# Kernel tuning notes

Measured on AMD Instinct MI355X. Metric: run time of the kernel, lower is better.

## Reference

```python
import jax, jax.numpy as jnp
import numpy as np

WINDOW_SIZE = 11
CHANNEL = 3
SIGMA = 1.5
C1 = 0.01 ** 2
C2 = 0.03 ** 2


def _create_window(window_size: int, channel: int) -> jnp.ndarray:
    coords = jnp.arange(window_size, dtype=jnp.float32) - window_size // 2
    g = jnp.exp(-coords ** 2 / (2 * SIGMA ** 2))
    g = g / g.sum()
    w2d = jnp.outer(g, g)  # [K, K]
    # depthwise conv kernel, OIHW with O=channel, I=1
    return jnp.broadcast_to(w2d, (channel, 1, window_size, window_size))


def _depthwise_conv(x, window):
    pad = WINDOW_SIZE // 2
    return jax.lax.conv_general_dilated(
        x, window,
        window_strides=(1, 1),
        padding=[(pad, pad), (pad, pad)],
        dimension_numbers=("NCHW", "OIHW", "NCHW"),
        feature_group_count=x.shape[1],
    )


def setup_inputs() -> dict:
    key = jax.random.key(0)
    k1, k2 = jax.random.split(key)
    pred = jax.random.uniform(k1, (16, 3, 512, 512), dtype=jnp.float32)
    target = jax.random.uniform(k2, (16, 3, 512, 512), dtype=jnp.float32)
    window = _create_window(WINDOW_SIZE, CHANNEL)
    return {"pred": pred, "target": target, "window": window}


def reference(pred, target, window):
    mu1 = _depthwise_conv(pred, window)
    mu2 = _depthwise_conv(target, window)
    mu1_sq = mu1 * mu1
    mu2_sq = mu2 * mu2
    mu1_mu2 = mu1 * mu2
    sigma1_sq = _depthwise_conv(pred * pred, window) - mu1_sq
    sigma2_sq = _depthwise_conv(target * target, window) - mu2_sq
    sigma12 = _depthwise_conv(pred * target, window) - mu1_mu2
    ssim_map = ((2 * mu1_mu2 + C1) * (2 * sigma12 + C2)) / (
        (mu1_sq + mu2_sq + C1) * (sigma1_sq + sigma2_sq + C2)
    )
    return 1.0 - ssim_map.mean()
```

## Files before the change

kernel.cpp:

```cpp
#include <hip/hip_runtime.h>

#define IMG_H 512
#define IMG_W 512
#define IMG_N (IMG_H * IMG_W)
#define NPLANES 48
#define TILE 64
#define XS 80
#define SSIM_C1 0.0001f
#define SSIM_C2 0.0009f

typedef _Float16 f16x2 __attribute__((ext_vector_type(2)));
typedef _Float16 f16x4 __attribute__((ext_vector_type(4)));
typedef _Float16 f16x8 __attribute__((ext_vector_type(8)));
typedef float    f32x4 __attribute__((ext_vector_type(4)));

__device__ __forceinline__ unsigned pk2(float a, float b) {
    return __builtin_bit_cast(unsigned,
        __builtin_amdgcn_cvt_pkrtz(a, b));
}
__device__ __forceinline__ f16x2 pk2h(float a, float b) {
    return __builtin_bit_cast(f16x2, __builtin_amdgcn_cvt_pkrtz(a, b));
}

template <bool CHECK>
__device__ __forceinline__ void stage_inputs(
    const float* __restrict__ pp, const float* __restrict__ tp,
    unsigned short* Xp, unsigned short* Xt,
    const int tid, const int base_r, const int base_c)
{
    float4   pb[7], tb[7];
    unsigned offv[7];
    bool     okv[7];
    #pragma unroll
    for (int i = 0; i < 7; ++i) {
        unsigned fi = (unsigned)tid + 256u * i;
        if (i == 6) fi = (fi < 1600u) ? fi : 0u;
        const unsigned ri = fi / 20u;
        const unsigned q  = fi - 20u * ri;
        int gr = base_r - 8 + (int)ri;
        int gc = base_c - 8 + 4 * (int)q;
        bool ok = true;
        if (CHECK) {
            ok = ((unsigned)gr < (unsigned)IMG_H) && ((unsigned)gc < (unsigned)IMG_W);
            gr = min(max(gr, 0), IMG_H - 1);
            gc = min(max(gc, 0), IMG_W - 4);
        }
        const int idx = gr * IMG_W + gc;
        pb[i]   = *(const float4*)(pp + idx);
        tb[i]   = *(const float4*)(tp + idx);
        okv[i]  = ok;
        offv[i] = ri * XS + 4u * q;
    }
    #pragma unroll
    for (int i = 0; i < 7; ++i) {
        float4 p4 = pb[i], t4 = tb[i];
        if (CHECK && !okv[i]) {
            p4 = make_float4(0.f, 0.f, 0.f, 0.f);
            t4 = make_float4(0.f, 0.f, 0.f, 0.f);
        }
        if (i < 6 || tid < 64) {
            *(uint2*)&Xp[offv[i]] = make_uint2(pk2(p4.x, p4.y), pk2(p4.z, p4.w));
            *(uint2*)&Xt[offv[i]] = make_uint2(pk2(t4.x, t4.y), pk2(t4.z, t4.w));
        }
    }
}

__global__ __launch_bounds__(256, 6) void ssim_mfma_kernel(
    const float* __restrict__ pred, const float* __restrict__ target,
    const float* __restrict__ window, float* __restrict__ partial)
{
    __shared__ __attribute__((aligned(16))) unsigned short Xp[80 * XS];
    __shared__ __attribute__((aligned(16))) unsigned short Xt[80 * XS];
    __shared__ unsigned short gfS[16];
    __shared__ float wsum[4];

    const int tid  = threadIdx.x;
    const int w    = tid >> 6;
    const int lane = tid & 63;
    const int n15  = lane & 15;
    const int quad = lane >> 4;

    if (tid < 16) {
        float gv = 0.f;
        if (tid < 11) {
            float s = 0.f;
            #pragma unroll
            for (int j = 0; j < 11; ++j) s += window[tid * 11 + j];
            gv = s;
        }
        const _Float16 hg = (_Float16)gv;
        gfS[tid] = __builtin_bit_cast(unsigned short, hg);
    }

    const int plane  = blockIdx.z;
    const int base_r = blockIdx.y * TILE;
    const int base_c = blockIdx.x * TILE;
    const float* pp = pred   + (size_t)plane * IMG_N;
    const float* tp = target + (size_t)plane * IMG_N;

    const bool interior = (blockIdx.x > 0) && (blockIdx.x < gridDim.x - 1) &&
                          (blockIdx.y > 0) && (blockIdx.y < gridDim.y - 1);
    if (interior) stage_inputs<false>(pp, tp, Xp, Xt, tid, base_r, base_c);
    else          stage_inputs<true >(pp, tp, Xp, Xt, tid, base_r, base_c);
    __syncthreads();

    uint4 wu;
    {
        unsigned wd[4];
        #pragma unroll
        for (int d = 0; d < 4; ++d) {
            const int t0 = 8 * quad + 2 * d - n15 - 3;
            const unsigned lo = gfS[((unsigned)t0       <= 10u) ? t0       : 11];
            const unsigned hi = gfS[((unsigned)(t0 + 1) <= 10u) ? (t0 + 1) : 11];
            wd[d] = lo | (hi << 16);
        }
        wu = make_uint4(wd[0], wd[1], wd[2], wd[3]);
    }
    const f16x8 wfrag = __builtin_bit_cast(f16x8, wu);

    f16x4 w0frag, w1frag;
    {
        unsigned a[2], b[2];
        #pragma unroll
        for (int d = 0; d < 2; ++d) {
            const int k0 = 4 * quad + 2 * d;
            const int a0 = k0 - n15 - 3,  a1 = a0 + 1;
            const int b0 = k0 - n15 + 13, b1 = b0 + 1;
            a[d] = gfS[((unsigned)a0 <= 10u) ? a0 : 11] |
                   ((unsigned)gfS[((unsigned)a1 <= 10u) ? a1 : 11] << 16);
            b[d] = gfS[((unsigned)b0 <= 10u) ? b0 : 11] |
                   ((unsigned)gfS[((unsigned)b1 <= 10u) ? b1 : 11] << 16);
        }
        w0frag = __builtin_bit_cast(f16x4, make_uint2(a[0], a[1]));
        w1frag = __builtin_bit_cast(f16x4, make_uint2(b[0], b[1]));
    }
    const f32x4 zero4 = {0.f, 0.f, 0.f, 0.f};

    auto h_tile = [&](int h, f16x4 (&P)[5]) {
        const int xoff = (16 * h + n15) * XS + 16 * w + 8 * quad;
        const f16x8 pu = *(const f16x8*)&Xp[xoff];
        const f16x8 tu = *(const f16x8*)&Xt[xoff];
        #pragma unroll
        for (int ch = 0; ch < 5; ++ch) {
            f16x8 au;
            if      (ch == 0) au = pu;
            else if (ch == 1) au = tu;
            else if (ch == 2) au = pu * pu;
            else if (ch == 3) au = tu * tu;
            else              au = pu * tu;
            const f32x4 hd = __builtin_amdgcn_mfma_f32_16x16x32_f16(
                au, wfrag, zero4, 0, 0, 0);
            const f16x2 l  = pk2h(hd[0], hd[1]);
            const f16x2 hh = pk2h(hd[2], hd[3]);
            P[ch] = f16x4{l.x, l.y, hh.x, hh.y};
        }
    };

    f16x4 Pprev[5], Pcur[5];
    h_tile(0, Pprev);

    float acc = 0.f;
    #pragma unroll
    for (int rt = 0; rt < 4; ++rt) {
        h_tile(rt + 1, Pcur);
        f32x4 s[5];
        #pragma unroll
        for (int ch = 0; ch < 5; ++ch) {
            const f32x4 t = __builtin_amdgcn_mfma_f32_16x16x16f16(
                w0frag, Pprev[ch], zero4, 0, 0, 0);
            s[ch] = __builtin_amdgcn_mfma_f32_16x16x16f16(
                w1frag, Pcur[ch], t, 0, 0, 0);
        }
        #pragma unroll
        for (int r = 0; r < 4; ++r) {
            const float mu1 = s[0][r], mu2 = s[1][r];
            const float e11 = s[2][r], e22 = s[3][r], e12 = s[4][r];
            const float mu1_sq = mu1 * mu1, mu2_sq = mu2 * mu2;
            const float mu1_mu2 = mu1 * mu2;
            const float s1  = e11 - mu1_sq;
            const float s2  = e22 - mu2_sq;
            const float s12 = e12 - mu1_mu2;
            const float num = (2.f * mu1_mu2 + SSIM_C1) * (2.f * s12 + SSIM_C2);
            const float den = (mu1_sq + mu2_sq + SSIM_C1) * (s1 + s2 + SSIM_C2);
            acc += num * __builtin_amdgcn_rcpf(den);
        }
        #pragma unroll
        for (int ch = 0; ch < 5; ++ch) Pprev[ch] = Pcur[ch];
    }

    #pragma unroll
    for (int off = 32; off > 0; off >>= 1)
        acc += __shfl_down(acc, off, 64);
    if (lane == 0) wsum[w] = acc;
    __syncthreads();
    if (tid == 0) {
        const int bid = blockIdx.x + gridDim.x * (blockIdx.y + gridDim.y * blockIdx.z);
        partial[bid] = wsum[0] + wsum[1] + wsum[2] + wsum[3];
    }
}

__global__ __launch_bounds__(256) void ssim_reduce_kernel(
    const float* __restrict__ partial, float* __restrict__ out)
{
    const int tid = threadIdx.x;
    float s = 0.f;
    #pragma unroll
    for (int k = 0; k < 12; ++k) s += partial[tid + 256 * k];
    double acc = (double)s;
    #pragma unroll
    for (int off = 32; off > 0; off >>= 1)
        acc += __shfl_down(acc, off, 64);
    __shared__ double wsumd[4];
    const int lane = tid & 63, wid = tid >> 6;
    if (lane == 0) wsumd[wid] = acc;
    __syncthreads();
    if (tid == 0) {
        const double total = wsumd[0] + wsumd[1] + wsumd[2] + wsumd[3];
        const double N = (double)NPLANES * IMG_H * IMG_W;
        out[0] = (float)(1.0 - total / N);
    }
}

extern "C" void kernel_launch(void* const* d_in, const int* in_sizes, int n_in,
                              void* d_out, int out_size, void* d_ws, size_t ws_size,
                              hipStream_t stream)
{
    const float* pred   = (const float*)d_in[0];
    const float* target = (const float*)d_in[1];
    const float* window = (const float*)d_in[2];
    float* out = (float*)d_out;
    float* partial = (float*)d_ws;

    dim3 grid(IMG_W / TILE, IMG_H / TILE, NPLANES);
    ssim_mfma_kernel<<<grid, 256, 0, stream>>>(pred, target, window, partial);
    ssim_reduce_kernel<<<1, 256, 0, stream>>>(partial, out);
}
```

Baseline: 128.8 us.

## Split input staging to overlap last rows' global loads with MFMA compute

Input staging is split into two phases. The first 1280 items (rows 0-63) are loaded and stored to LDS up front. The loads for the last 16 rows are issued after the first barrier, and their LDS stores are deferred until the first three row tiles have been computed. This overlaps part of the global-memory latency with MFMA work, at the cost of an extra barrier, more live registers, and a duplicated code body for the interior and border cases.

```diff
diff --git a/kernel.cpp b/kernel.cpp
--- a/kernel.cpp
+++ b/kernel.cpp
@@ -23,85 +23,53 @@
 }
 
 template <bool CHECK>
-__device__ __forceinline__ void stage_inputs(
+__device__ __forceinline__ void load_item(
     const float* __restrict__ pp, const float* __restrict__ tp,
-    unsigned short* Xp, unsigned short* Xt,
-    const int tid, const int base_r, const int base_c)
-{
-    float4   pb[7], tb[7];
-    unsigned offv[7];
-    bool     okv[7];
-    #pragma unroll
-    for (int i = 0; i < 7; ++i) {
-        unsigned fi = (unsigned)tid + 256u * i;
-        if (i == 6) fi = (fi < 1600u) ? fi : 0u;
-        const unsigned ri = fi / 20u;
-        const unsigned q  = fi - 20u * ri;
-        int gr = base_r - 8 + (int)ri;
-        int gc = base_c - 8 + 4 * (int)q;
-        bool ok = true;
-        if (CHECK) {
-            ok = ((unsigned)gr < (unsigned)IMG_H) && ((unsigned)gc < (unsigned)IMG_W);
-            gr = min(max(gr, 0), IMG_H - 1);
-            gc = min(max(gc, 0), IMG_W - 4);
-        }
-        const int idx = gr * IMG_W + gc;
-        pb[i]   = *(const float4*)(pp + idx);
-        tb[i]   = *(const float4*)(tp + idx);
-        okv[i]  = ok;
-        offv[i] = ri * XS + 4u * q;
-    }
-    #pragma unroll
-    for (int i = 0; i < 7; ++i) {
-        float4 p4 = pb[i], t4 = tb[i];
-        if (CHECK && !okv[i]) {
-            p4 = make_float4(0.f, 0.f, 0.f, 0.f);
-            t4 = make_float4(0.f, 0.f, 0.f, 0.f);
-        }
-        if (i < 6 || tid < 64) {
-            *(uint2*)&Xp[offv[i]] = make_uint2(pk2(p4.x, p4.y), pk2(p4.z, p4.w));
-            *(uint2*)&Xt[offv[i]] = make_uint2(pk2(t4.x, t4.y), pk2(t4.z, t4.w));
-        }
-    }
-}
-
-__global__ __launch_bounds__(256, 6) void ssim_mfma_kernel(
-    const float* __restrict__ pred, const float* __restrict__ target,
-    const float* __restrict__ window, float* __restrict__ partial)
-{
-    __shared__ __attribute__((aligned(16))) unsigned short Xp[80 * XS];
-    __shared__ __attribute__((aligned(16))) unsigned short Xt[80 * XS];
-    __shared__ unsigned short gfS[16];
-    __shared__ float wsum[4];
-
-    const int tid  = threadIdx.x;
-    const int w    = tid >> 6;
-    const int lane = tid & 63;
-    const int n15  = lane & 15;
-    const int quad = lane >> 4;
-
-    if (tid < 16) {
-        float gv = 0.f;
-        if (tid < 11) {
-            float s = 0.f;
-            #pragma unroll
-            for (int j = 0; j < 11; ++j) s += window[tid * 11 + j];
-            gv = s;
-        }
-        const _Float16 hg = (_Float16)gv;
-        gfS[tid] = __builtin_bit_cast(unsigned short, hg);
-    }
-
-    const int plane  = blockIdx.z;
-    const int base_r = blockIdx.y * TILE;
-    const int base_c = blockIdx.x * TILE;
-    const float* pp = pred   + (size_t)plane * IMG_N;
-    const float* tp = target + (size_t)plane * IMG_N;
-
-    const bool interior = (blockIdx.x > 0) && (blockIdx.x < gridDim.x - 1) &&
-                          (blockIdx.y > 0) && (blockIdx.y < gridDim.y - 1);
-    if (interior) stage_inputs<false>(pp, tp, Xp, Xt, tid, base_r, base_c);
-    else          stage_inputs<true >(pp, tp, Xp, Xt, tid, base_r, base_c);
+    const unsigned fi, const int base_r, const int base_c,
+    float4& p4, float4& t4, unsigned& off, bool& ok)
+{
+    const unsigned ri = fi / 20u, q = fi - 20u * ri;
+    int gr = base_r - 8 + (int)ri;
+    int gc = base_c - 8 + 4 * (int)q;
+    ok = true;
+    if (CHECK) {
+        ok = ((unsigned)gr < (unsigned)IMG_H) && ((unsigned)gc < (unsigned)IMG_W);
+        gr = min(max(gr, 0), IMG_H - 1);
+        gc = min(max(gc, 0), IMG_W - 4);
+    }
+    const int idx = gr * IMG_W + gc;
+    p4  = *(const float4*)(pp + idx);
+    t4  = *(const float4*)(tp + idx);
+    off = ri * XS + 4u * q;
+}
+
+__device__ __forceinline__ void store_item(
+    unsigned short* Xp, unsigned short* Xt, const unsigned off,
+    float4 p4, float4 t4, const bool zero)
+{
+    if (zero) {
+        p4 = make_float4(0.f, 0.f, 0.f, 0.f);
+        t4 = make_float4(0.f, 0.f, 0.f, 0.f);
+    }
+    *(uint2*)&Xp[off] = make_uint2(pk2(p4.x, p4.y), pk2(p4.z, p4.w));
+    *(uint2*)&Xt[off] = make_uint2(pk2(t4.x, t4.y), pk2(t4.z, t4.w));
+}
+
+template <bool CHECK>
+__device__ __forceinline__ float ssim_body(
+    const float* __restrict__ pp, const float* __restrict__ tp,
+    unsigned short* Xp, unsigned short* Xt, const unsigned short* gfS,
+    const int tid, const int cw, const int n15, const int quad,
+    const int base_r, const int base_c)
+{
+    float4   pa[5], ta[5];
+    unsigned offA[5];
+    bool     okA[5];
+    #pragma unroll
+    for (int i = 0; i < 5; ++i)
+        load_item<CHECK>(pp, tp, (unsigned)tid + 256u * i, base_r, base_c,
+                         pa[i], ta[i], offA[i], okA[i]);
+
     __syncthreads();
 
     uint4 wu;
@@ -136,8 +104,25 @@
     }
     const f32x4 zero4 = {0.f, 0.f, 0.f, 0.f};
 
+    #pragma unroll
+    for (int i = 0; i < 5; ++i)
+        store_item(Xp, Xt, offA[i], pa[i], ta[i], CHECK && !okA[i]);
+
+    __syncthreads();
+
+    float4   pb0, tb0, pb1, tb1;
+    unsigned offB0, offB1;
+    bool     okB0, okB1;
+    {
+        const unsigned fi0 = 1280u + (unsigned)tid;
+        unsigned       fi1 = 1536u + (unsigned)tid;
+        if (fi1 >= 1600u) fi1 = 1280u;
+        load_item<CHECK>(pp, tp, fi0, base_r, base_c, pb0, tb0, offB0, okB0);
+        load_item<CHECK>(pp, tp, fi1, base_r, base_c, pb1, tb1, offB1, okB1);
+    }
+
     auto h_tile = [&](int h, f16x4 (&P)[5]) {
-        const int xoff = (16 * h + n15) * XS + 16 * w + 8 * quad;
+        const int xoff = (16 * h + n15) * XS + 16 * cw + 8 * quad;
         const f16x8 pu = *(const f16x8*)&Xp[xoff];
         const f16x8 tu = *(const f16x8*)&Xt[xoff];
         #pragma unroll
@@ -156,20 +141,15 @@
         }
     };
 
-    f16x4 Pprev[5], Pcur[5];
-    h_tile(0, Pprev);
-
     float acc = 0.f;
-    #pragma unroll
-    for (int rt = 0; rt < 4; ++rt) {
-        h_tile(rt + 1, Pcur);
+    auto v_ssim = [&](const f16x4 (&Pp)[5], const f16x4 (&Pc)[5]) {
         f32x4 s[5];
         #pragma unroll
         for (int ch = 0; ch < 5; ++ch) {
             const f32x4 t = __builtin_amdgcn_mfma_f32_16x16x16f16(
-                w0frag, Pprev[ch], zero4, 0, 0, 0);
+                w0frag, Pp[ch], zero4, 0, 0, 0);
             s[ch] = __builtin_amdgcn_mfma_f32_16x16x16f16(
-                w1frag, Pcur[ch], t, 0, 0, 0);
+                w1frag, Pc[ch], t, 0, 0, 0);
         }
         #pragma unroll
         for (int r = 0; r < 4; ++r) {
@@ -184,14 +164,76 @@
             const float den = (mu1_sq + mu2_sq + SSIM_C1) * (s1 + s2 + SSIM_C2);
             acc += num * __builtin_amdgcn_rcpf(den);
         }
+    };
+
+    f16x4 Pprev[5], Pcur[5];
+    h_tile(0, Pprev);
+    #pragma unroll
+    for (int rt = 0; rt < 3; ++rt) {
+        h_tile(rt + 1, Pcur);
+        v_ssim(Pprev, Pcur);
         #pragma unroll
         for (int ch = 0; ch < 5; ++ch) Pprev[ch] = Pcur[ch];
     }
+
+    store_item(Xp, Xt, offB0, pb0, tb0, CHECK && !okB0);
+    if (tid < 64)
+        store_item(Xp, Xt, offB1, pb1, tb1, CHECK && !okB1);
+
+    __syncthreads();
+
+    h_tile(4, Pcur);
+    v_ssim(Pprev, Pcur);
+    return acc;
+}
+
+__global__ __launch_bounds__(256, 6) void ssim_mfma_kernel(
+    const float* __restrict__ pred, const float* __restrict__ target,
+    const float* __restrict__ window, float* __restrict__ partial)
+{
+    __shared__ __attribute__((aligned(16))) unsigned short Xp[80 * XS];
+    __shared__ __attribute__((aligned(16))) unsigned short Xt[80 * XS];
+    __shared__ unsigned short gfS[16];
+    __shared__ float wsum[4];
+
+    const int tid  = threadIdx.x;
+    const int cw   = tid >> 6;
+    const int lane = tid & 63;
+    const int n15  = lane & 15;
+    const int quad = lane >> 4;
+
+    if (tid < 16) {
+        float gv = 0.f;
+        if (tid < 11) {
+            float s = 0.f;
+            #pragma unroll
+            for (int j = 0; j < 11; ++j) s += window[tid * 11 + j];
+            gv = s;
+        }
+        const _Float16 hg = (_Float16)gv;
+        gfS[tid] = __builtin_bit_cast(unsigned short, hg);
+    }
+
+    const int plane  = blockIdx.z;
+    const int base_r = blockIdx.y * TILE;
+    const int base_c = blockIdx.x * TILE;
+    const float* pp = pred   + (size_t)plane * IMG_N;
+    const float* tp = target + (size_t)plane * IMG_N;
+
+    const bool interior = (blockIdx.x > 0) && (blockIdx.x < gridDim.x - 1) &&
+                          (blockIdx.y > 0) && (blockIdx.y < gridDim.y - 1);
+    float acc;
+    if (interior)
+        acc = ssim_body<false>(pp, tp, Xp, Xt, gfS, tid, cw, n15, quad,
+                               base_r, base_c);
+    else
+        acc = ssim_body<true >(pp, tp, Xp, Xt, gfS, tid, cw, n15, quad,
+                               base_r, base_c);
 
     #pragma unroll
     for (int off = 32; off > 0; off >>= 1)
         acc += __shfl_down(acc, off, 64);
-    if (lane == 0) wsum[w] = acc;
+    if (lane == 0) wsum[cw] = acc;
     __syncthreads();
     if (tid == 0) {
         const int bid = blockIdx.x + gridDim.x * (blockIdx.y + gridDim.y * blockIdx.z);
```

New measurement: 151.8 us. +17.8%, slower.
